# Kernel tuning notes

Hardware: AMD Instinct MI355X
Metric: run time of the kernel (lower is better)

Reference implementation:

```python
import jax, jax.numpy as jnp
from jax import lax
import numpy as np

LOGZERO = -(65504.0 ** 2)  # -torch.finfo(float16).min**2


def setup_inputs() -> dict:
    key = jax.random.key(0)
    ks = jax.random.split(key, 5)
    B, T, D, V, CB, Ly = 32, 512, 512, 4096, 30, 4
    x = jax.random.normal(ks[0], (B, T, D), jnp.float32)
    W = jax.random.normal(ks[1], (V, D), jnp.float32) * 0.02
    b = jax.random.normal(ks[2], (V,), jnp.float32) * 0.02
    xl = jnp.full((B,), T, jnp.int32)
    y = jax.random.randint(ks[3], (B, Ly), 1, V)  # partial hypothesis (last token used)
    # unique candidate ids per row (exclude blank=0) to avoid duplicate-scatter ambiguity
    scores = jax.random.uniform(ks[4], (B, V - 1))
    ctc_beam_idx = jnp.argsort(scores, axis=1)[:, :CB] + 1
    return {"x": x, "W": W, "b": b, "xl": xl, "y": y,
            "ctc_beam_idx": ctc_beam_idx, "blank": 0, "eos": V - 1}


def reference(x, W, b, xl, y, ctc_beam_idx, blank, eos):
    B, T, D = x.shape
    V = W.shape[0]
    CB = ctc_beam_idx.shape[1]
    # forward(): Linear + log_softmax  -> (B, T, V)
    logp = jax.nn.log_softmax(jnp.einsum("btd,vd->btv", x, W) + b, axis=-1)
    # preProcess(): lastP[1] = cumsum of blank logprob over time, lastP[0] = logzero
    blank_lp = logp[:, :, blank]                     # (B, T)
    lastP1 = jnp.cumsum(blank_lp, axis=1).T          # (T, B)
    lastP0 = jnp.full((T, B), LOGZERO, logp.dtype)
    lastPsum = jnp.logaddexp(lastP0, lastP1)         # (T, B)
    # cState.select / bState.select -> candidate and blank scores per beam hyp
    Xn = jnp.take_along_axis(logp, ctc_beam_idx[:, None, :], axis=2)  # (B, T, CB)
    Xn = Xn.transpose(1, 0, 2)                                        # (T, B, CB)
    Xb = jnp.broadcast_to(blank_lp.T[:, :, None], Xn.shape)           # (T, B, CB)
    # prefP: lastPsum everywhere, lastP[1] where candidate == last prediction
    same = (y[:, -1][:, None] == ctc_beam_idx)                        # (B, CB)
    prefP = jnp.where(same[None], lastP1[:, :, None], lastPsum[:, :, None])  # (T, B, CB)
    Ly = y.shape[1]
    start = min(Ly, T - 1)
    loop_start = max(start, 1)
    Pn0 = jnp.full((B, CB), LOGZERO, logp.dtype)
    Pb0 = jnp.full((B, CB), LOGZERO, logp.dtype)
    if start == 0:
        Pn0 = Xn[0]
    def step(carry, inp):
        Pn_prev, Pb_prev = carry
        pref_prev, xn_t, xb_t = inp
        Pn = jnp.logaddexp(Pn_prev, pref_prev) + xn_t
        Pb = jnp.logaddexp(Pn_prev, Pb_prev) + xb_t
        return (Pn, Pb), (Pn, Pb)
    _, (Pn_seq, Pb_seq) = lax.scan(
        step, (Pn0, Pb0),
        (prefP[loop_start - 1:T - 1], Xn[loop_start:], Xb[loop_start:]))
    if start == 0:  # prepend the preset t=0 entry
        Pn_seq = jnp.concatenate([Pn0[None], Pn_seq], axis=0)
        Pb_seq = jnp.concatenate([Pb0[None], Pb_seq], axis=0)
    # curP over t in [start, T)
    curP_t = jnp.logaddexp(Pn_seq, Pb_seq)                            # (T-start, B, CB)
    t_idx = jnp.arange(start, T)
    valid = xl[None, :] > t_idx[:, None]                              # (T-start, B)
    curP_t = jnp.where(valid[:, :, None], curP_t, LOGZERO)
    curP = jax.nn.logsumexp(curP_t, axis=0)                           # (B, CB)
    # scatter into vocab; initial self.prefP == 0.0
    finalP = jnp.full((B, V), LOGZERO, curP.dtype)
    finalP = finalP.at[jnp.arange(B)[:, None], ctc_beam_idx].set(curP)
    # eos score: lastPsum at final valid frame only
    ar = jnp.arange(T)
    maskBT = xl[:, None] > ar[None, :]
    mask0 = (xl - 1)[:, None] > ar[None, :]
    lps = jnp.where(maskBT & ~mask0, lastPsum.T, 0.0)                 # (B, T)
    finalP = finalP.at[:, eos].set(jnp.sum(lps, axis=1))
    finalP = finalP.at[:, blank].set(LOGZERO)
    return finalP
```

## Files before the change

### kernel.cpp

```cpp
#include <hip/hip_runtime.h>
#include <hip/hip_fp8.h>

#define LOGZERO -4290774016.0f
#define L2E 1.4426950408889634f
#define LN2 0.6931471805599453f

constexpr int Bb = 32, Tt = 512, Dd = 512, Vv = 4096;
constexpr int BT = Bb * Tt;

typedef __attribute__((ext_vector_type(4)))  float f32x4;
typedef __attribute__((ext_vector_type(16))) float f32x16;
typedef __attribute__((ext_vector_type(4)))  int   i32x4;
typedef __attribute__((ext_vector_type(8)))  int   i32x8;

#define GLOBAL_AS __attribute__((address_space(1)))
#define LDS_AS    __attribute__((address_space(3)))

__device__ __forceinline__ float fexp2(float x) { return __builtin_amdgcn_exp2f(x); }
__device__ __forceinline__ float flog2(float x) { return __builtin_amdgcn_logf(x); }

__device__ __forceinline__ unsigned cvt4_fp8(float4 v, float s) {
#if __has_builtin(__builtin_amdgcn_cvt_pk_fp8_f32)
  int p = __builtin_amdgcn_cvt_pk_fp8_f32(v.x * s, v.y * s, 0, false);
  p = __builtin_amdgcn_cvt_pk_fp8_f32(v.z * s, v.w * s, p, true);
  return (unsigned)p;
#else
  unsigned b0 = __hip_cvt_float_to_fp8(v.x * s, __HIP_SATFINITE, __HIP_E4M3);
  unsigned b1 = __hip_cvt_float_to_fp8(v.y * s, __HIP_SATFINITE, __HIP_E4M3);
  unsigned b2 = __hip_cvt_float_to_fp8(v.z * s, __HIP_SATFINITE, __HIP_E4M3);
  unsigned b3 = __hip_cvt_float_to_fp8(v.w * s, __HIP_SATFINITE, __HIP_E4M3);
  return b0 | (b1 << 8) | (b2 << 16) | (b3 << 24);
#endif
}

__device__ __forceinline__ float lg2add(float a, float b) {
  float mx = fmaxf(a, b);
  float d  = fabsf(a - b);
  return mx + flog2(1.0f + fexp2(-d));
}

__global__ __launch_bounds__(256) void kPre(const float* __restrict__ x,
                                            const float* __restrict__ W,
                                            unsigned char* __restrict__ Xfp,
                                            unsigned char* __restrict__ Wp) {
  __shared__ unsigned char T[16384];
  const int tid = threadIdx.x, bid = blockIdx.x;
  const bool isX = bid < 512;
  const float* srcF;
  float scale;
  int cb = 0, half = 0;
  if (isX) {
    srcF = x + (size_t)bid * 32 * Dd;
    scale = 1.0f;
  } else {
    int idx = bid - 512;
    cb = idx >> 1; half = idx & 1;
    srcF = W + ((size_t)cb * 64 + half * 32) * Dd;
    scale = 16.0f;
  }

  #pragma unroll
  for (int p = 0; p < 16; ++p) {
    int f = p * 256 + tid;
    int r = f >> 7;
    int cf = f & 127;
    int c = cf >> 2, m = cf & 3;
    float4 v = *(const float4*)(srcF + (size_t)f * 4);
    unsigned o = cvt4_fp8(v, scale);
    *(unsigned*)(T + ((r * 32 + (c ^ r)) * 16 + m * 4)) = o;
  }
  __syncthreads();

  if (isX) {
    unsigned char* dst = Xfp + (size_t)bid * 16384;
    #pragma unroll
    for (int u = 0; u < 4; ++u) {
      int s = u * 256 + tid;
      int r = s & 31, khalf = (s >> 5) & 1, h = (s >> 6) & 1, kb = s >> 7;
      int c = kb * 4 + khalf * 2 + h;
      uint4 o = *(const uint4*)(T + (r * 32 + (c ^ r)) * 16);
      *(uint4*)(dst + (size_t)s * 16) = o;
    }
  } else {
    unsigned char* dst = Wp + (size_t)cb * 32768;
    #pragma unroll
    for (int u = 0; u < 4; ++u) {
      int lsl = u * 256 + tid;
      int r = lsl & 31, khalf = (lsl >> 5) & 1, h = (lsl >> 6) & 1, kb = lsl >> 7;
      int c = kb * 4 + khalf * 2 + h;
      int s = kb * 256 + half * 128 + h * 64 + khalf * 32 + r;
      uint4 o = *(const uint4*)(T + (r * 32 + (c ^ r)) * 16);
      *(uint4*)(dst + (size_t)s * 16) = o;
    }
  }
}

__global__ __launch_bounds__(256, 6) void kA(const unsigned char* __restrict__ Xfp,
                                             const unsigned char* __restrict__ Wp,
                                             const float* __restrict__ bias,
                                             const int* __restrict__ beam,
                                             const int* __restrict__ blankp,
                                             float* __restrict__ Spart,
                                             float* __restrict__ selL,
                                             int CB) {
  __shared__ unsigned char Ald[16384];
  __shared__ float Spw[4][32];
  __shared__ int   selv[31];
  __shared__ float selb[31];

  const int tid = threadIdx.x;
  const int tileN = blockIdx.x & 15;
  const int tileM = blockIdx.x >> 4;
  const int row0 = tileM * 32, col0 = tileN * 256;
  const int bb = row0 >> 9;
  const int lane = tid & 63, w = tid >> 6;
  const int l31 = lane & 31, hi = lane >> 5;

  if (tid < 31) {
    int v = (tid == 0) ? *blankp : beam[bb * CB + tid - 1];
    selv[tid] = v;
    selb[tid] = bias[v];
  }

  const unsigned char* src = Xfp + (size_t)tileM * 16384;
  #pragma unroll
  for (int i = 0; i < 4; ++i) {
    int off = (w * 4 + i) * 1024;
    __builtin_amdgcn_global_load_lds((const GLOBAL_AS void*)(src + off + lane * 16),
                                     (LDS_AS void*)(Ald + off), 16, 0, 0);
  }
  __syncthreads();

  const int colw = col0 + w * 64;
  const int cb = tileN * 4 + w;

  f32x16 acc[2];
  #pragma unroll
  for (int ct = 0; ct < 2; ++ct)
    #pragma unroll
    for (int r = 0; r < 16; ++r) acc[ct][r] = 0.f;

  const unsigned char* wpB = Wp + (size_t)cb * 32768 + lane * 16;

  i32x8 bc[2];
  #pragma unroll
  for (int ct = 0; ct < 2; ++ct) {
    i32x4 lo = *(const i32x4*)(wpB + (ct * 2) * 1024);
    i32x4 hx = *(const i32x4*)(wpB + (ct * 2 + 1) * 1024);
    bc[ct] = __builtin_shufflevector(lo, hx, 0, 1, 2, 3, 4, 5, 6, 7);
  }

  #pragma unroll
  for (int kb = 0; kb < 8; ++kb) {
    i32x8 af;
    {
      i32x4 lo = *(const i32x4*)&Ald[(kb * 2) * 1024 + lane * 16];
      i32x4 hx = *(const i32x4*)&Ald[(kb * 2 + 1) * 1024 + lane * 16];
      af = __builtin_shufflevector(lo, hx, 0, 1, 2, 3, 4, 5, 6, 7);
    }
    i32x8 bn[2];
    const int kn = (kb < 7) ? kb + 1 : 7;
    #pragma unroll
    for (int ct = 0; ct < 2; ++ct) {
      i32x4 lo = *(const i32x4*)(wpB + (kn * 4 + ct * 2) * 1024);
      i32x4 hx = *(const i32x4*)(wpB + (kn * 4 + ct * 2 + 1) * 1024);
      bn[ct] = __builtin_shufflevector(lo, hx, 0, 1, 2, 3, 4, 5, 6, 7);
    }
    #pragma unroll
    for (int ct = 0; ct < 2; ++ct)
      acc[ct] = __builtin_amdgcn_mfma_scale_f32_32x32x64_f8f6f4(
          af, bc[ct], acc[ct],
          0, 0,
          0, 0x7f7f7f7f,
          0, 0x7b7b7b7b);
    bc[0] = bn[0]; bc[1] = bn[1];
  }

  float bvl[2];
  #pragma unroll
  for (int ct = 0; ct < 2; ++ct)
    bvl[ct] = bias[colw + ct * 32 + l31] * L2E;

  #pragma unroll
  for (int reg = 0; reg < 16; ++reg) {
    float s = fexp2(acc[0][reg] * L2E + bvl[0]) +
              fexp2(acc[1][reg] * L2E + bvl[1]);
    s += __shfl_xor(s, 1, 64);
    s += __shfl_xor(s, 2, 64);
    s += __shfl_xor(s, 4, 64);
    s += __shfl_xor(s, 8, 64);
    s += __shfl_xor(s, 16, 64);
    if (l31 == 0)
      Spw[w][(reg & 3) + 8 * (reg >> 2) + 4 * hi] = s;
  }
  __syncthreads();
  if (tid < 32) {
    float p = Spw[0][tid] + Spw[1][tid] + Spw[2][tid] + Spw[3][tid];
    Spart[(size_t)tileN * BT + row0 + tid] = p;
  }

  const int tbase = row0 & 511;
  #pragma unroll 1
  for (int s = 0; s < 31; ++s) {
    const int vsel = __builtin_amdgcn_readfirstlane(selv[s]);
    const int local = vsel - colw;
    if (local >= 0 && local < 32) {
      const float bvs = selb[s];
      if (l31 == local) {
        #pragma unroll
        for (int reg = 0; reg < 16; ++reg) {
          int t = tbase + (reg & 3) + 8 * (reg >> 2) + 4 * hi;
          selL[((size_t)bb * Tt + t) * 31 + s] = acc[0][reg] + bvs;
        }
      }
    } else if (local >= 32 && local < 64) {
      const float bvs = selb[s];
      if (l31 == (local & 31)) {
        #pragma unroll
        for (int reg = 0; reg < 16; ++reg) {
          int t = tbase + (reg & 3) + 8 * (reg >> 2) + 4 * hi;
          selL[((size_t)bb * Tt + t) * 31 + s] = acc[1][reg] + bvs;
        }
      }
    }
  }
}

__global__ __launch_bounds__(256) void kC(const float* __restrict__ selL,
                                          const float* __restrict__ Spart,
                                          const int* __restrict__ xl,
                                          const int* __restrict__ beam,
                                          const int* __restrict__ blankp,
                                          const int* __restrict__ eosp,
                                          float* __restrict__ out,
                                          int Ly, int CB) {
  __shared__ float sl[Tt * 31];
  __shared__ float lgS[Tt];
  __shared__ float lastP1[Tt];
  const int b = blockIdx.x, tid = threadIdx.x;

  for (int tt = tid; tt < Tt; tt += 256) {
    float s = 0.f;
    #pragma unroll
    for (int n = 0; n < 16; ++n) s += Spart[(size_t)n * BT + b * Tt + tt];
    lgS[tt] = flog2(s);
  }
  __syncthreads();
  for (int i = tid; i < Tt * 31; i += 256) {
    int t = i / 31;
    sl[i] = selL[(size_t)b * Tt * 31 + i] * L2E - lgS[t];
  }
  __syncthreads();

  float* orow = out + (size_t)b * Vv;
  for (int i = tid; i < Vv; i += 256) orow[i] = LOGZERO;

  const int xlb = xl[b];
  float curP = LOGZERO;
  if (tid < 64) {
    const int lane = tid;
    float vloc[8];
    float run = 0.f;
    #pragma unroll
    for (int u = 0; u < 8; ++u) {
      int t = lane * 8 + u;
      float bl = sl[t * 31];
      run += bl;
      vloc[u] = run;
    }
    float inc = run;
    #pragma unroll
    for (int off = 1; off < 64; off <<= 1) {
      float o = __shfl_up(inc, off, 64);
      if (lane >= off) inc += o;
    }
    float excl = inc - run;
    #pragma unroll
    for (int u = 0; u < 8; ++u) lastP1[lane * 8 + u] = vloc[u] + excl;

    const int kk = (lane < CB) ? lane : (CB - 1);
    const float LOG2ZERO = LOGZERO * L2E;
    float Pn = LOG2ZERO, Pb = LOG2ZERO;
    float mrun = -3.0e38f, srun = 0.0f;
    int start = (Ly < Tt - 1) ? Ly : (Tt - 1);
    if (start == 0) {
      Pn = sl[1 + kk];
      float vv = (0 < xlb) ? lg2add(Pn, Pb) : LOG2ZERO;
      float nm = fmaxf(mrun, vv);
      srun = srun * fexp2(mrun - nm) + fexp2(vv - nm);
      mrun = nm;
    }
    int t0 = (start > 1) ? start : 1;
    float xn_c = sl[t0 * 31 + 1 + kk];
    float xb_c = sl[t0 * 31];
    float pf_c = lastP1[t0 - 1];
    #pragma unroll 2
    for (int t = t0; t < Tt; ++t) {
      float xn_n = 0.f, xb_n = 0.f, pf_n = 0.f;
      if (t + 1 < Tt) {
        xn_n = sl[(t + 1) * 31 + 1 + kk];
        xb_n = sl[(t + 1) * 31];
        pf_n = lastP1[t];
      }
      float Pn2 = lg2add(Pn, pf_c) + xn_c;
      float Pb2 = lg2add(Pn, Pb) + xb_c;
      Pn = Pn2; Pb = Pb2;
      float vv = (t < xlb) ? lg2add(Pn, Pb) : LOG2ZERO;
      float nm = fmaxf(mrun, vv);
      srun = srun * fexp2(mrun - nm) + fexp2(vv - nm);
      mrun = nm;
      xn_c = xn_n; xb_c = xb_n; pf_c = pf_n;
    }
    curP = (mrun + flog2(srun)) * LN2;
  }
  __syncthreads();

  if (tid < 64) {
    if (tid < CB) orow[beam[b * CB + tid]] = curP;
  }
  __syncthreads();
  if (tid == 0) {
    float eosv = (xlb >= 1) ? lastP1[xlb - 1] * LN2 : 0.0f;
    orow[*eosp] = eosv;
    orow[*blankp] = LOGZERO;
  }
}

extern "C" void kernel_launch(void* const* d_in, const int* in_sizes, int n_in,
                              void* d_out, int out_size, void* d_ws, size_t ws_size,
                              hipStream_t stream) {
  (void)n_in; (void)out_size; (void)ws_size;
  const float* x    = (const float*)d_in[0];
  const float* W    = (const float*)d_in[1];
  const float* bias = (const float*)d_in[2];
  const int* xl     = (const int*)d_in[3];
  const int* beam   = (const int*)d_in[5];
  const int* blankp = (const int*)d_in[6];
  const int* eosp   = (const int*)d_in[7];
  const int Ly = in_sizes[4] / Bb;
  const int CB = in_sizes[5] / Bb;

  float* Spart = (float*)d_ws;
  float* selL  = (float*)((char*)d_ws + (size_t)0x100000);
  unsigned char* Xfp = (unsigned char*)((char*)d_ws + (size_t)0x400000);
  unsigned char* Wp  = (unsigned char*)((char*)d_ws + (size_t)0xC00000);
  float* outf = (float*)d_out;

  kPre<<<640, 256, 0, stream>>>(x, W, Xfp, Wp);
  kA<<<8192, 256, 0, stream>>>(Xfp, Wp, bias, beam, blankp, Spart, selL, CB);
  kC<<<Bb, 256, 0, stream>>>(selL, Spart, xl, beam, blankp, eosp, outf, Ly, CB);
}
```

Before: 233.0 us.

## Double GEMM M-tile to 64 rows so each W fragment feeds two MFMAs

The logits GEMM kernel now handles 64 rows per block instead of 32. Each wave holds a 2x2 set of 32x32 accumulators, so every fp8 W fragment loaded from global memory is reused across two row tiles, and the grid shrinks to half as many blocks. LDS use doubles and the launch-bounds occupancy hint drops from 6 to 4, which raises register pressure and lowers occupancy. The k-loop is also left un-unrolled, and the recurrence kernel's conditional prefetch becomes a clamped unconditional load.

Measured after the change: 232.9 us. About the same (-0.0%).

```diff
diff --git a/kernel.cpp b/kernel.cpp
--- a/kernel.cpp
+++ b/kernel.cpp
@@ -37,6 +37,12 @@
   float mx = fmaxf(a, b);
   float d  = fabsf(a - b);
   return mx + flog2(1.0f + fexp2(-d));
+}
+
+__device__ __forceinline__ i32x8 ld2(const unsigned char* p) {
+  i32x4 lo = *(const i32x4*)p;
+  i32x4 hx = *(const i32x4*)(p + 1024);
+  return __builtin_shufflevector(lo, hx, 0, 1, 2, 3, 4, 5, 6, 7);
 }
 
 __global__ __launch_bounds__(256) void kPre(const float* __restrict__ x,
@@ -95,7 +101,7 @@
   }
 }
 
-__global__ __launch_bounds__(256, 6) void kA(const unsigned char* __restrict__ Xfp,
+__global__ __launch_bounds__(256, 4) void kA(const unsigned char* __restrict__ Xfp,
                                              const unsigned char* __restrict__ Wp,
                                              const float* __restrict__ bias,
                                              const int* __restrict__ beam,
@@ -103,15 +109,15 @@
                                              float* __restrict__ Spart,
                                              float* __restrict__ selL,
                                              int CB) {
-  __shared__ unsigned char Ald[16384];
-  __shared__ float Spw[4][32];
+  __shared__ unsigned char Ald[32768];
+  __shared__ float Spw[4][64];
   __shared__ int   selv[31];
   __shared__ float selb[31];
 
   const int tid = threadIdx.x;
   const int tileN = blockIdx.x & 15;
   const int tileM = blockIdx.x >> 4;
-  const int row0 = tileM * 32, col0 = tileN * 256;
+  const int row0 = tileM * 64, col0 = tileN * 256;
   const int bb = row0 >> 9;
   const int lane = tid & 63, w = tid >> 6;
   const int l31 = lane & 31, hi = lane >> 5;
@@ -122,10 +128,10 @@
     selb[tid] = bias[v];
   }
 
-  const unsigned char* src = Xfp + (size_t)tileM * 16384;
-  #pragma unroll
-  for (int i = 0; i < 4; ++i) {
-    int off = (w * 4 + i) * 1024;
+  const unsigned char* src = Xfp + (size_t)tileM * 32768;
+  #pragma unroll
+  for (int i = 0; i < 8; ++i) {
+    int off = (w * 8 + i) * 1024;
     __builtin_amdgcn_global_load_lds((const GLOBAL_AS void*)(src + off + lane * 16),
                                      (LDS_AS void*)(Ald + off), 16, 0, 0);
   }
@@ -134,45 +140,41 @@
   const int colw = col0 + w * 64;
   const int cb = tileN * 4 + w;
 
-  f32x16 acc[2];
+  f32x16 acc[2][2];
   #pragma unroll
   for (int ct = 0; ct < 2; ++ct)
     #pragma unroll
-    for (int r = 0; r < 16; ++r) acc[ct][r] = 0.f;
+    for (int mt = 0; mt < 2; ++mt)
+      #pragma unroll
+      for (int r = 0; r < 16; ++r) acc[ct][mt][r] = 0.f;
 
   const unsigned char* wpB = Wp + (size_t)cb * 32768 + lane * 16;
+  const unsigned char* aB  = Ald + lane * 16;
 
   i32x8 bc[2];
-  #pragma unroll
-  for (int ct = 0; ct < 2; ++ct) {
-    i32x4 lo = *(const i32x4*)(wpB + (ct * 2) * 1024);
-    i32x4 hx = *(const i32x4*)(wpB + (ct * 2 + 1) * 1024);
-    bc[ct] = __builtin_shufflevector(lo, hx, 0, 1, 2, 3, 4, 5, 6, 7);
-  }
-
-  #pragma unroll
+  bc[0] = ld2(wpB);
+  bc[1] = ld2(wpB + 2048);
+
+  #pragma unroll 1
   for (int kb = 0; kb < 8; ++kb) {
-    i32x8 af;
-    {
-      i32x4 lo = *(const i32x4*)&Ald[(kb * 2) * 1024 + lane * 16];
-      i32x4 hx = *(const i32x4*)&Ald[(kb * 2 + 1) * 1024 + lane * 16];
-      af = __builtin_shufflevector(lo, hx, 0, 1, 2, 3, 4, 5, 6, 7);
-    }
     i32x8 bn[2];
     const int kn = (kb < 7) ? kb + 1 : 7;
-    #pragma unroll
-    for (int ct = 0; ct < 2; ++ct) {
-      i32x4 lo = *(const i32x4*)(wpB + (kn * 4 + ct * 2) * 1024);
-      i32x4 hx = *(const i32x4*)(wpB + (kn * 4 + ct * 2 + 1) * 1024);
-      bn[ct] = __builtin_shufflevector(lo, hx, 0, 1, 2, 3, 4, 5, 6, 7);
-    }
-    #pragma unroll
-    for (int ct = 0; ct < 2; ++ct)
-      acc[ct] = __builtin_amdgcn_mfma_scale_f32_32x32x64_f8f6f4(
-          af, bc[ct], acc[ct],
-          0, 0,
-          0, 0x7f7f7f7f,
-          0, 0x7b7b7b7b);
+    bn[0] = ld2(wpB + kn * 4096);
+    bn[1] = ld2(wpB + kn * 4096 + 2048);
+    {
+      i32x8 af0 = ld2(aB + kb * 2048);
+      acc[0][0] = __builtin_amdgcn_mfma_scale_f32_32x32x64_f8f6f4(
+          af0, bc[0], acc[0][0], 0, 0, 0, 0x7f7f7f7f, 0, 0x7b7b7b7b);
+      acc[1][0] = __builtin_amdgcn_mfma_scale_f32_32x32x64_f8f6f4(
+          af0, bc[1], acc[1][0], 0, 0, 0, 0x7f7f7f7f, 0, 0x7b7b7b7b);
+    }
+    {
+      i32x8 af1 = ld2(aB + 16384 + kb * 2048);
+      acc[0][1] = __builtin_amdgcn_mfma_scale_f32_32x32x64_f8f6f4(
+          af1, bc[0], acc[0][1], 0, 0, 0, 0x7f7f7f7f, 0, 0x7b7b7b7b);
+      acc[1][1] = __builtin_amdgcn_mfma_scale_f32_32x32x64_f8f6f4(
+          af1, bc[1], acc[1][1], 0, 0, 0, 0x7f7f7f7f, 0, 0x7b7b7b7b);
+    }
     bc[0] = bn[0]; bc[1] = bn[1];
   }
 
@@ -182,19 +184,22 @@
     bvl[ct] = bias[colw + ct * 32 + l31] * L2E;
 
   #pragma unroll
-  for (int reg = 0; reg < 16; ++reg) {
-    float s = fexp2(acc[0][reg] * L2E + bvl[0]) +
-              fexp2(acc[1][reg] * L2E + bvl[1]);
-    s += __shfl_xor(s, 1, 64);
-    s += __shfl_xor(s, 2, 64);
-    s += __shfl_xor(s, 4, 64);
-    s += __shfl_xor(s, 8, 64);
-    s += __shfl_xor(s, 16, 64);
-    if (l31 == 0)
-      Spw[w][(reg & 3) + 8 * (reg >> 2) + 4 * hi] = s;
-  }
-  __syncthreads();
-  if (tid < 32) {
+  for (int mt = 0; mt < 2; ++mt) {
+    #pragma unroll
+    for (int reg = 0; reg < 16; ++reg) {
+      float s = fexp2(acc[0][mt][reg] * L2E + bvl[0]) +
+                fexp2(acc[1][mt][reg] * L2E + bvl[1]);
+      s += __shfl_xor(s, 1, 64);
+      s += __shfl_xor(s, 2, 64);
+      s += __shfl_xor(s, 4, 64);
+      s += __shfl_xor(s, 8, 64);
+      s += __shfl_xor(s, 16, 64);
+      if (l31 == 0)
+        Spw[w][mt * 32 + (reg & 3) + 8 * (reg >> 2) + 4 * hi] = s;
+    }
+  }
+  __syncthreads();
+  if (tid < 64) {
     float p = Spw[0][tid] + Spw[1][tid] + Spw[2][tid] + Spw[3][tid];
     Spart[(size_t)tileN * BT + row0 + tid] = p;
   }
@@ -208,19 +213,23 @@
       const float bvs = selb[s];
       if (l31 == local) {
         #pragma unroll
-        for (int reg = 0; reg < 16; ++reg) {
-          int t = tbase + (reg & 3) + 8 * (reg >> 2) + 4 * hi;
-          selL[((size_t)bb * Tt + t) * 31 + s] = acc[0][reg] + bvs;
-        }
+        for (int mt = 0; mt < 2; ++mt)
+          #pragma unroll
+          for (int reg = 0; reg < 16; ++reg) {
+            int t = tbase + mt * 32 + (reg & 3) + 8 * (reg >> 2) + 4 * hi;
+            selL[((size_t)bb * Tt + t) * 31 + s] = acc[0][mt][reg] + bvs;
+          }
       }
     } else if (local >= 32 && local < 64) {
       const float bvs = selb[s];
       if (l31 == (local & 31)) {
         #pragma unroll
-        for (int reg = 0; reg < 16; ++reg) {
-          int t = tbase + (reg & 3) + 8 * (reg >> 2) + 4 * hi;
-          selL[((size_t)bb * Tt + t) * 31 + s] = acc[1][reg] + bvs;
-        }
+        for (int mt = 0; mt < 2; ++mt)
+          #pragma unroll
+          for (int reg = 0; reg < 16; ++reg) {
+            int t = tbase + mt * 32 + (reg & 3) + 8 * (reg >> 2) + 4 * hi;
+            selL[((size_t)bb * Tt + t) * 31 + s] = acc[1][mt][reg] + bvs;
+          }
       }
     }
   }
@@ -296,12 +305,10 @@
     float pf_c = lastP1[t0 - 1];
     #pragma unroll 2
     for (int t = t0; t < Tt; ++t) {
-      float xn_n = 0.f, xb_n = 0.f, pf_n = 0.f;
-      if (t + 1 < Tt) {
-        xn_n = sl[(t + 1) * 31 + 1 + kk];
-        xb_n = sl[(t + 1) * 31];
-        pf_n = lastP1[t];
-      }
+      int tn = (t + 1 < Tt) ? (t + 1) : (Tt - 1);
+      float xn_n = sl[tn * 31 + 1 + kk];
+      float xb_n = sl[tn * 31];
+      float pf_n = lastP1[tn - 1];
       float Pn2 = lg2add(Pn, pf_c) + xn_c;
       float Pb2 = lg2add(Pn, Pb) + xb_c;
       Pn = Pn2; Pb = Pb2;
@@ -347,6 +354,6 @@
   float* outf = (float*)d_out;
 
   kPre<<<640, 256, 0, stream>>>(x, W, Xfp, Wp);
-  kA<<<8192, 256, 0, stream>>>(Xfp, Wp, bias, beam, blankp, Spart, selL, CB);
+  kA<<<4096, 256, 0, stream>>>(Xfp, Wp, bias, beam, blankp, Spart, selL, CB);
   kC<<<Bb, 256, 0, stream>>>(selL, Spart, xl, beam, blankp, eosp, outf, Ly, CB);
 }
```
